# Optimization experiments

Hardware: AMD Instinct MI355X
Metric: run time of the kernel (lower is better)

The kernel has to match this reference:

```python
import jax, jax.numpy as jnp
import numpy as np

N, D = 131072, 512
G, NG = 512, 256  # G groups of equal size NG, contiguous; N == G*NG
MARGIN, LAMBDA_CD, LAMBDA_CDD, LAMBDA_PCC, K_MARGIN = 2.0, 0.0, 1.0, 1.0, 0.02
EPS = 1e-6


def setup_inputs() -> dict:
    key = jax.random.key(0)
    k1, k2, k3, k4 = jax.random.split(key, 4)
    z_r = jax.random.normal(k1, (N, D), jnp.float32)
    z_r = z_r / jnp.linalg.norm(z_r, axis=-1, keepdims=True)
    z_v = jax.random.normal(k2, (N, D), jnp.float32)
    z_v = z_v / jnp.linalg.norm(z_v, axis=-1, keepdims=True)
    labels = jax.random.randint(k3, (N,), 0, 2)
    groups = jnp.repeat(jnp.arange(G), NG)  # contiguous equal-size groups
    var_lens = jax.random.randint(k4, (N,), 0, 10000)
    return {"z_r": z_r, "z_v": z_v, "labels": labels, "groups": groups, "var_lens": var_lens}


def reference(z_r, z_v, labels, groups, var_lens):
    # cosine distance per pair: [N]
    d = 1.0 - jnp.sum(z_r * z_v, axis=-1)

    mb = (labels == 0).astype(d.dtype)
    mp = (labels == 1).astype(d.dtype)
    nb, npos = mb.sum(), mp.sum()
    db_mean = jnp.sum(d * mb) / jnp.maximum(nb, 1.0)
    dp_mean = jnp.sum(d * mp) / jnp.maximum(npos, 1.0)

    l_cd = jnp.where(nb > 0, db_mean, 0.0)
    l_cdd = jnp.where((nb > 0) & (npos > 0),
                      jax.nn.relu(MARGIN + db_mean - dp_mean), 0.0)

    # --- per-group losses, vectorized over G equal-size contiguous groups ---
    d_g = d.reshape(G, NG)                                   # [G, n_g]
    v_g = var_lens.reshape(G, NG).astype(d.dtype)            # [G, n_g]

    # Pearson-style z-score matching loss (torch std is unbiased, ddof=1)
    v_std = jnp.std(v_g, axis=1, ddof=1)
    d_std = jnp.std(d_g, axis=1, ddof=1)
    v_z = (v_g - v_g.mean(axis=1, keepdims=True)) / (v_std + EPS)[:, None]
    d_z = (d_g - d_g.mean(axis=1, keepdims=True)) / (d_std + EPS)[:, None]
    corr_loss = jnp.mean((v_z - d_z) ** 2, axis=1)
    corr_loss = jnp.where((v_std > 0) & (d_std > 0), corr_loss, 0.0)

    # sort each group by var_len
    order = jnp.argsort(v_g, axis=1)
    v_s = jnp.take_along_axis(v_g, order, axis=1)            # [G, n_g]
    d_s = jnp.take_along_axis(d_g, order, axis=1)            # [G, n_g]

    # neighbor monotonicity violation
    neigh_viol = jnp.mean(jax.nn.relu(d_s[:, :-1] - d_s[:, 1:] + K_MARGIN), axis=1)

    # pairwise rank loss: dv[g,i,j] = v_s[g,j] - v_s[g,i] (matches torch unsqueeze(0)-unsqueeze(1))
    dv = v_s[:, None, :] - v_s[:, :, None]                   # [G, n_g, n_g]
    dd = d_s[:, None, :] - d_s[:, :, None]                   # [G, n_g, n_g]
    mask = (dv > 0).astype(d.dtype)
    cnt = mask.sum(axis=(1, 2))
    pair_sum = jnp.sum(jax.nn.relu(K_MARGIN - dd) * mask, axis=(1, 2))
    rank_loss = jnp.where(cnt > 0, pair_sum / jnp.maximum(cnt, 1.0), 0.0)

    group_loss = corr_loss + neigh_viol + rank_loss          # [G]
    # size-weighted sum; all groups have equal size NG -> plain mean
    l_pcc = jnp.mean(group_loss)

    total = LAMBDA_CD * l_cd + LAMBDA_CDD * l_cdd + LAMBDA_PCC * l_pcc
    return total, l_cdd, l_pcc, d
```

## Files before the change

### kernel.cpp

```cpp
#include <hip/hip_runtime.h>

#define NTOT   131072
#define DIMV   512
#define GCNT   512
#define NGRP   256
#define KMARG  0.02f
#define CMARG  2.0f
#define EPSC   1e-6f

__device__ __forceinline__ float wave_sum(float v) {
#pragma unroll
  for (int off = 32; off; off >>= 1) v += __shfl_down(v, off, 64);
  return v;
}

template <int NW>
__device__ __forceinline__ float block_sum(float v, float* red) {
  const int t = threadIdx.x;
  v = wave_sum(v);
  __syncthreads();
  if ((t & 63) == 0) red[t >> 6] = v;
  __syncthreads();
  float s = 0.0f;
#pragma unroll
  for (int i = 0; i < NW; ++i) s += red[i];
  return s;
}

__global__ __launch_bounds__(256) void dot_kernel(const float* __restrict__ zr,
                                                  const float* __restrict__ zv,
                                                  float* __restrict__ dout) {
  const int wave = threadIdx.x >> 6;
  const int lane = threadIdx.x & 63;
  const int row  = (blockIdx.x << 2) + wave;
  const float4* r = (const float4*)zr + ((size_t)row << 7);
  const float4* v = (const float4*)zv + ((size_t)row << 7);
  float4 a0 = r[lane];
  float4 b0 = v[lane];
  float4 a1 = r[lane + 64];
  float4 b1 = v[lane + 64];
  float s = a0.x * b0.x + a0.y * b0.y + a0.z * b0.z + a0.w * b0.w +
            a1.x * b1.x + a1.y * b1.y + a1.z * b1.z + a1.w * b1.w;
  s = wave_sum(s);
  if (lane == 0) dout[row] = 1.0f - s;
}

__global__ __launch_bounds__(256) void group_kernel(const float* __restrict__ d,
                                                    const int* __restrict__ labels,
                                                    const int* __restrict__ varl,
                                                    float* __restrict__ gout) {
  __shared__ float red[4];
  __shared__ int   skey[NGRP];
  __shared__ float sval[NGRP];
  const int g = blockIdx.x, t = threadIdx.x;
  const int idx = g * NGRP + t;
  const float dv  = d[idx];
  const int   vli = varl[idx];
  const float vv  = (float)vli;
  const int   lab = labels[idx];

  const float sb = block_sum<4>((lab == 0) ? dv : 0.0f, red);
  const float cb = block_sum<4>((lab == 0) ? 1.0f : 0.0f, red);
  const float sp = block_sum<4>((lab == 1) ? dv : 0.0f, red);
  const float cp = block_sum<4>((lab == 1) ? 1.0f : 0.0f, red);

  const float mv = block_sum<4>(vv, red) * (1.0f / NGRP);
  const float md = block_sum<4>(dv, red) * (1.0f / NGRP);
  const float vdev = vv - mv, ddev = dv - md;
  const float vvar = block_sum<4>(vdev * vdev, red) * (1.0f / (NGRP - 1));
  const float dvar = block_sum<4>(ddev * ddev, red) * (1.0f / (NGRP - 1));
  const float vstd = sqrtf(vvar), dstd = sqrtf(dvar);
  const float vz = vdev / (vstd + EPSC), dz = ddev / (dstd + EPSC);
  float corr = block_sum<4>((vz - dz) * (vz - dz), red) * (1.0f / NGRP);
  corr = (vstd > 0.0f && dstd > 0.0f) ? corr : 0.0f;

  skey[t] = (vli << 8) | t;
  sval[t] = dv;
  __syncthreads();
  for (int k = 2; k <= NGRP; k <<= 1) {
    for (int j = k >> 1; j > 0; j >>= 1) {
      const int ixj = t ^ j;
      if (ixj > t) {
        const int k1 = skey[t], k2 = skey[ixj];
        const bool up = ((t & k) == 0);
        if (up ? (k1 > k2) : (k1 < k2)) {
          const float v1 = sval[t], v2 = sval[ixj];
          skey[t] = k2; skey[ixj] = k1;
          sval[t] = v2; sval[ixj] = v1;
        }
      }
      __syncthreads();
    }
  }

  float nv = 0.0f;
  if (t < NGRP - 1) nv = fmaxf(sval[t] - sval[t + 1] + KMARG, 0.0f);
  const float neigh = block_sum<4>(nv, red) * (1.0f / (NGRP - 1));

  const int   vi = skey[t] >> 8;
  const float di = sval[t];
  float ps = 0.0f, pc = 0.0f;
  for (int jj = 0; jj < NGRP; ++jj) {
    const int   vj = skey[jj] >> 8;
    const float dj = sval[jj];
    if (vj > vi) {
      pc += 1.0f;
      ps += fmaxf(KMARG - (dj - di), 0.0f);
    }
  }
  const float PS = block_sum<4>(ps, red);
  const float PC = block_sum<4>(pc, red);
  const float rank = (PC > 0.0f) ? PS / fmaxf(PC, 1.0f) : 0.0f;

  if (t == 0) {
    gout[g]            = corr + neigh + rank;
    gout[GCNT + g]     = sb;
    gout[2 * GCNT + g] = sp;
    gout[3 * GCNT + g] = cb;
    gout[4 * GCNT + g] = cp;
  }
}

__global__ __launch_bounds__(512) void final_kernel(const float* __restrict__ gout,
                                                    float* __restrict__ out) {
  __shared__ float red[8];
  const int t = threadIdx.x;
  const float L  = block_sum<8>(gout[t], red);
  const float SB = block_sum<8>(gout[GCNT + t], red);
  const float SP = block_sum<8>(gout[2 * GCNT + t], red);
  const float CB = block_sum<8>(gout[3 * GCNT + t], red);
  const float CP = block_sum<8>(gout[4 * GCNT + t], red);
  if (t == 0) {
    const float db = SB / fmaxf(CB, 1.0f);
    const float dp = SP / fmaxf(CP, 1.0f);
    const float l_cdd = (CB > 0.0f && CP > 0.0f) ? fmaxf(CMARG + db - dp, 0.0f) : 0.0f;
    const float l_pcc = L * (1.0f / GCNT);
    out[0] = l_cdd + l_pcc;
    out[1] = l_cdd;
    out[2] = l_pcc;
  }
}

extern "C" void kernel_launch(void* const* d_in, const int* in_sizes, int n_in,
                              void* d_out, int out_size, void* d_ws, size_t ws_size,
                              hipStream_t stream) {
  const float* zr     = (const float*)d_in[0];
  const float* zv     = (const float*)d_in[1];
  const int*   labels = (const int*)d_in[2];
  const int*   varl   = (const int*)d_in[4];
  float* out  = (float*)d_out;
  float* dvec = out + 3;
  float* gws  = (float*)d_ws;

  dot_kernel<<<NTOT / 4, 256, 0, stream>>>(zr, zv, dvec);
  group_kernel<<<GCNT, 256, 0, stream>>>(dvec, labels, varl, gws);
  final_kernel<<<1, 512, 0, stream>>>(gws, out);
}
```

Before: 129.7 us.

## Replace bitonic sort with rank counting, batch block reductions, widen dot rows

The group kernel drops the shared-memory bitonic sort. Each thread now finds its position by counting smaller keys during the pairwise pass that already exists. The many separate block reductions become three batched multi-value reductions. The correlation loss is computed algebraically from sums of squares and the cross term. Positive-label sums are derived from totals instead of being reduced separately. The dot kernel has each wave handle two rows with nontemporal loads. Together these cut sync barriers and the sort cost, with the risk of slightly different float rounding in the algebraic correlation.

```diff
diff --git a/kernel.cpp b/kernel.cpp
--- a/kernel.cpp
+++ b/kernel.cpp
@@ -8,23 +8,35 @@
 #define CMARG  2.0f
 #define EPSC   1e-6f
 
+typedef float f4 __attribute__((ext_vector_type(4)));
+
+template <int NW, int M>
+__device__ __forceinline__ void block_sum_m(float* v, float* red) {
+  const int t = threadIdx.x;
+#pragma unroll
+  for (int m = 0; m < M; ++m) {
+#pragma unroll
+    for (int off = 32; off; off >>= 1) v[m] += __shfl_down(v[m], off, 64);
+  }
+  __syncthreads();
+  if ((t & 63) == 0) {
+#pragma unroll
+    for (int m = 0; m < M; ++m) red[(t >> 6) * M + m] = v[m];
+  }
+  __syncthreads();
+#pragma unroll
+  for (int m = 0; m < M; ++m) {
+    float s = 0.0f;
+#pragma unroll
+    for (int i = 0; i < NW; ++i) s += red[i * M + m];
+    v[m] = s;
+  }
+}
+
 __device__ __forceinline__ float wave_sum(float v) {
 #pragma unroll
   for (int off = 32; off; off >>= 1) v += __shfl_down(v, off, 64);
   return v;
-}
-
-template <int NW>
-__device__ __forceinline__ float block_sum(float v, float* red) {
-  const int t = threadIdx.x;
-  v = wave_sum(v);
-  __syncthreads();
-  if ((t & 63) == 0) red[t >> 6] = v;
-  __syncthreads();
-  float s = 0.0f;
-#pragma unroll
-  for (int i = 0; i < NW; ++i) s += red[i];
-  return s;
 }
 
 __global__ __launch_bounds__(256) void dot_kernel(const float* __restrict__ zr,
@@ -32,105 +44,97 @@
                                                   float* __restrict__ dout) {
   const int wave = threadIdx.x >> 6;
   const int lane = threadIdx.x & 63;
-  const int row  = (blockIdx.x << 2) + wave;
-  const float4* r = (const float4*)zr + ((size_t)row << 7);
-  const float4* v = (const float4*)zv + ((size_t)row << 7);
-  float4 a0 = r[lane];
-  float4 b0 = v[lane];
-  float4 a1 = r[lane + 64];
-  float4 b1 = v[lane + 64];
-  float s = a0.x * b0.x + a0.y * b0.y + a0.z * b0.z + a0.w * b0.w +
-            a1.x * b1.x + a1.y * b1.y + a1.z * b1.z + a1.w * b1.w;
-  s = wave_sum(s);
-  if (lane == 0) dout[row] = 1.0f - s;
+  const int row0 = ((blockIdx.x << 2) + wave) << 1;
+  const f4* r = (const f4*)zr + ((size_t)row0 << 7);
+  const f4* v = (const f4*)zv + ((size_t)row0 << 7);
+  f4 a0 = __builtin_nontemporal_load(r + lane);
+  f4 b0 = __builtin_nontemporal_load(v + lane);
+  f4 a1 = __builtin_nontemporal_load(r + lane + 64);
+  f4 b1 = __builtin_nontemporal_load(v + lane + 64);
+  f4 a2 = __builtin_nontemporal_load(r + lane + 128);
+  f4 b2 = __builtin_nontemporal_load(v + lane + 128);
+  f4 a3 = __builtin_nontemporal_load(r + lane + 192);
+  f4 b3 = __builtin_nontemporal_load(v + lane + 192);
+  f4 p = a0 * b0 + a1 * b1;
+  f4 q = a2 * b2 + a3 * b3;
+  float s0 = wave_sum(p.x + p.y + p.z + p.w);
+  float s1 = wave_sum(q.x + q.y + q.z + q.w);
+  if (lane == 0) {
+    dout[row0]     = 1.0f - s0;
+    dout[row0 + 1] = 1.0f - s1;
+  }
 }
 
 __global__ __launch_bounds__(256) void group_kernel(const float* __restrict__ d,
                                                     const int* __restrict__ labels,
                                                     const int* __restrict__ varl,
                                                     float* __restrict__ gout) {
-  __shared__ float red[4];
-  __shared__ int   skey[NGRP];
-  __shared__ float sval[NGRP];
+  __shared__ float  red[4 * 4];
+  __shared__ float2 skv[NGRP];
+  __shared__ float  sdat[NGRP];
   const int g = blockIdx.x, t = threadIdx.x;
   const int idx = g * NGRP + t;
   const float dv  = d[idx];
-  const int   vli = varl[idx];
-  const float vv  = (float)vli;
+  const float vv  = (float)varl[idx];
   const int   lab = labels[idx];
 
-  const float sb = block_sum<4>((lab == 0) ? dv : 0.0f, red);
-  const float cb = block_sum<4>((lab == 0) ? 1.0f : 0.0f, red);
-  const float sp = block_sum<4>((lab == 1) ? dv : 0.0f, red);
-  const float cp = block_sum<4>((lab == 1) ? 1.0f : 0.0f, red);
+  skv[t] = make_float2(vv, dv);
 
-  const float mv = block_sum<4>(vv, red) * (1.0f / NGRP);
-  const float md = block_sum<4>(dv, red) * (1.0f / NGRP);
+  float sA[4] = {dv, vv, (lab == 0) ? dv : 0.0f, (lab == 0) ? 1.0f : 0.0f};
+  block_sum_m<4, 4>(sA, red);
+  const float sumd = sA[0], sumv = sA[1], sb = sA[2], cb = sA[3];
+  const float md = sumd * (1.0f / NGRP), mv = sumv * (1.0f / NGRP);
+
   const float vdev = vv - mv, ddev = dv - md;
-  const float vvar = block_sum<4>(vdev * vdev, red) * (1.0f / (NGRP - 1));
-  const float dvar = block_sum<4>(ddev * ddev, red) * (1.0f / (NGRP - 1));
-  const float vstd = sqrtf(vvar), dstd = sqrtf(dvar);
-  const float vz = vdev / (vstd + EPSC), dz = ddev / (dstd + EPSC);
-  float corr = block_sum<4>((vz - dz) * (vz - dz), red) * (1.0f / NGRP);
+  float sB[3] = {vdev * vdev, ddev * ddev, vdev * ddev};
+  block_sum_m<4, 3>(sB, red);
+  const float svv = sB[0], sdd = sB[1], svd = sB[2];
+  const float vstd = sqrtf(svv * (1.0f / (NGRP - 1)));
+  const float dstd = sqrtf(sdd * (1.0f / (NGRP - 1)));
+  const float iv = 1.0f / (vstd + EPSC), id = 1.0f / (dstd + EPSC);
+  float corr = (svv * iv * iv + sdd * id * id - 2.0f * svd * iv * id) * (1.0f / NGRP);
   corr = (vstd > 0.0f && dstd > 0.0f) ? corr : 0.0f;
 
-  skey[t] = (vli << 8) | t;
-  sval[t] = dv;
   __syncthreads();
-  for (int k = 2; k <= NGRP; k <<= 1) {
-    for (int j = k >> 1; j > 0; j >>= 1) {
-      const int ixj = t ^ j;
-      if (ixj > t) {
-        const int k1 = skey[t], k2 = skey[ixj];
-        const bool up = ((t & k) == 0);
-        if (up ? (k1 > k2) : (k1 < k2)) {
-          const float v1 = sval[t], v2 = sval[ixj];
-          skey[t] = k2; skey[ixj] = k1;
-          sval[t] = v2; sval[ixj] = v1;
-        }
-      }
-      __syncthreads();
+  int rank = 0;
+  float pc = 0.0f, ps = 0.0f;
+  const float pre = KMARG + dv;
+  for (int j = 0; j < NGRP; ++j) {
+    const float2 kv = skv[j];
+    const float vj = kv.x, dj = kv.y;
+    if (vj > vv) {
+      pc += 1.0f;
+      ps += fmaxf(pre - dj, 0.0f);
     }
+    rank += (vj < vv || (vj == vv && j < t)) ? 1 : 0;
   }
+  sdat[rank] = dv;
+  __syncthreads();
+  const float nv = (t < NGRP - 1) ? fmaxf(sdat[t] - sdat[t + 1] + KMARG, 0.0f) : 0.0f;
 
-  float nv = 0.0f;
-  if (t < NGRP - 1) nv = fmaxf(sval[t] - sval[t + 1] + KMARG, 0.0f);
-  const float neigh = block_sum<4>(nv, red) * (1.0f / (NGRP - 1));
-
-  const int   vi = skey[t] >> 8;
-  const float di = sval[t];
-  float ps = 0.0f, pc = 0.0f;
-  for (int jj = 0; jj < NGRP; ++jj) {
-    const int   vj = skey[jj] >> 8;
-    const float dj = sval[jj];
-    if (vj > vi) {
-      pc += 1.0f;
-      ps += fmaxf(KMARG - (dj - di), 0.0f);
-    }
-  }
-  const float PS = block_sum<4>(ps, red);
-  const float PC = block_sum<4>(pc, red);
-  const float rank = (PC > 0.0f) ? PS / fmaxf(PC, 1.0f) : 0.0f;
+  float sC[3] = {ps, pc, nv};
+  block_sum_m<4, 3>(sC, red);
+  const float rank_loss = (sC[1] > 0.0f) ? sC[0] / fmaxf(sC[1], 1.0f) : 0.0f;
+  const float neigh = sC[2] * (1.0f / (NGRP - 1));
 
   if (t == 0) {
-    gout[g]            = corr + neigh + rank;
+    gout[g]            = corr + neigh + rank_loss;
     gout[GCNT + g]     = sb;
-    gout[2 * GCNT + g] = sp;
-    gout[3 * GCNT + g] = cb;
-    gout[4 * GCNT + g] = cp;
+    gout[2 * GCNT + g] = cb;
+    gout[3 * GCNT + g] = sumd;
   }
 }
 
 __global__ __launch_bounds__(512) void final_kernel(const float* __restrict__ gout,
                                                     float* __restrict__ out) {
-  __shared__ float red[8];
+  __shared__ float red[8 * 4];
   const int t = threadIdx.x;
-  const float L  = block_sum<8>(gout[t], red);
-  const float SB = block_sum<8>(gout[GCNT + t], red);
-  const float SP = block_sum<8>(gout[2 * GCNT + t], red);
-  const float CB = block_sum<8>(gout[3 * GCNT + t], red);
-  const float CP = block_sum<8>(gout[4 * GCNT + t], red);
+  float s[4] = {gout[t], gout[GCNT + t], gout[2 * GCNT + t], gout[3 * GCNT + t]};
+  block_sum_m<8, 4>(s, red);
   if (t == 0) {
+    const float L = s[0], SB = s[1], CB = s[2], SumD = s[3];
+    const float SP = SumD - SB;
+    const float CP = (float)NTOT - CB;
     const float db = SB / fmaxf(CB, 1.0f);
     const float dp = SP / fmaxf(CP, 1.0f);
     const float l_cdd = (CB > 0.0f && CP > 0.0f) ? fmaxf(CMARG + db - dp, 0.0f) : 0.0f;
@@ -152,7 +156,7 @@
   float* dvec = out + 3;
   float* gws  = (float*)d_ws;
 
-  dot_kernel<<<NTOT / 4, 256, 0, stream>>>(zr, zv, dvec);
+  dot_kernel<<<NTOT / 8, 256, 0, stream>>>(zr, zv, dvec);
   group_kernel<<<GCNT, 256, 0, stream>>>(dvec, labels, varl, gws);
   final_kernel<<<1, 512, 0, stream>>>(gws, out);
 }
```

Measured after the change: 114.5 us. -11.7%, faster.
